# Performance work log

Hardware: AMD Instinct MI355X
Metric: run time of the kernel (lower is better)

## Reference

```python
import jax, jax.numpy as jnp
import numpy as np


def setup_inputs() -> dict:
    key = jax.random.key(0)
    ks = jax.random.split(key, 10)
    N, S, H = 500000, 128, 64
    s = lambda k, shape, fan_in: jax.random.normal(k, shape, dtype=jnp.float32) / np.sqrt(fan_in)
    return {
        "my_state": jax.random.normal(ks[0], (S,), dtype=jnp.float32),
        "neighbor_states": jax.random.normal(ks[1], (N, S), dtype=jnp.float32),
        "embed_w": s(ks[2], (S, H), S),
        "embed_b": s(ks[3], (H,), S),
        "key_w": s(ks[4], (H, H), H),
        "key_b": s(ks[5], (H,), H),
        "query_w": s(ks[6], (S + H, H), S + H),
        "query_b": s(ks[7], (H,), S + H),
        "attn_w": s(ks[8], (2 * H, 1), 2 * H),
        "attn_b": s(ks[9], (1,), 2 * H),
    }


def reference(my_state, neighbor_states, embed_w, embed_b, key_w, key_b,
              query_w, query_b, attn_w, attn_b):
    H = embed_w.shape[1]
    # per-neighbor embeddings and keys: [N, H]
    emb = neighbor_states @ embed_w + embed_b
    keys = emb @ key_w + key_b
    # query from own state + mean neighbor embedding: [H]
    mean_emb = emb.mean(axis=0)
    query = jnp.concatenate([my_state, mean_emb], axis=-1) @ query_w + query_b
    # attention_net(cat(query, key)) split so we never materialize [N, 2H]
    wq, wk = attn_w[:H, 0], attn_w[H:, 0]
    scores = keys @ wk + (query @ wq + attn_b[0])  # [N]
    attention_weights = jax.nn.softmax(scores, axis=0)  # [N]
    weighted_embedding = attention_weights @ emb  # [H]
    return weighted_embedding, attention_weights
```

## Files before the change

kernel.cpp:

```cpp
#include <hip/hip_runtime.h>
#include <math.h>


#define S_DIM 128
#define H_DIM 64
#define NBLK  2048

__global__ void k_precompute_u(const float* __restrict__ embed_w,
                               const float* __restrict__ key_w,
                               const float* __restrict__ attn_w,
                               float* __restrict__ u)
{
    __shared__ float kv[H_DIM];
    const int t = threadIdx.x;
    if (t < H_DIM) {
        float acc = 0.f;
        #pragma unroll 8
        for (int j = 0; j < H_DIM; ++j) acc += key_w[t * H_DIM + j] * attn_w[H_DIM + j];
        kv[t] = acc;
    }
    __syncthreads();
    float acc = 0.f;
    #pragma unroll 8
    for (int h = 0; h < H_DIM; ++h) acc += embed_w[t * H_DIM + h] * kv[h];
    u[t] = acc;
}

__global__ __launch_bounds__(256) void k_pass1(
    const float* __restrict__ X,
    const float* __restrict__ u,
    float* __restrict__ scores_out,
    float* __restrict__ pz,
    float* __restrict__ pt_t,
    int N)
{
    const int tid  = threadIdx.x;
    const int lane = tid & 63;
    const int li   = lane & 31;
    const int half = lane >> 5;
    const int w    = tid >> 6;

    const float4 u4 = *(const float4*)(u + 4 * li);

    const int pairs = (N + 1) >> 1;
    const int start = (int)(((long long)blockIdx.x       * pairs) / NBLK);
    const int end   = (int)(((long long)(blockIdx.x + 1) * pairs) / NBLK);

    auto loadp = [&](int p) -> float4 {
        int row = 2 * p + half;
        row = row < N ? row : N - 1;
        return *(const float4*)(X + (size_t)row * S_DIM + 4 * li);
    };

    float  Za = 0.f, Zb = 0.f;
    float4 ta = make_float4(0.f, 0.f, 0.f, 0.f);
    float4 tb = make_float4(0.f, 0.f, 0.f, 0.f);

    auto proc = [&](const float4& x, int p, float& Z, float4& t) {
        float pp = x.x * u4.x + x.y * u4.y + x.z * u4.z + x.w * u4.w;
        pp += __shfl_xor(pp, 1);
        pp += __shfl_xor(pp, 2);
        pp += __shfl_xor(pp, 4);
        pp += __shfl_xor(pp, 8);
        pp += __shfl_xor(pp, 16);
        const int  row = 2 * p + half;
        const bool v   = (p < end) && (row < N);
        if (li == 0 && v) scores_out[row] = pp;
        const float e = v ? __expf(pp) : 0.f;
        Z   += e;
        t.x += e * x.x;
        t.y += e * x.y;
        t.z += e * x.z;
        t.w += e * x.w;
    };

    int p = start + w;
    float4 xa = loadp(p);
    float4 xb = loadp(p + 4);
    while (p < end) {
        float4 na = loadp(p + 8);
        float4 nb = loadp(p + 12);
        proc(xa, p,     Za, ta);
        proc(xb, p + 4, Zb, tb);
        xa = na; xb = nb; p += 8;
    }

    const float  Z = Za + Zb;
    const float4 t = make_float4(ta.x + tb.x, ta.y + tb.y, ta.z + tb.z, ta.w + tb.w);

    __shared__ float sT[8][S_DIM];
    __shared__ float sZ[8];
    const int hs = w * 2 + half;
    sT[hs][4 * li + 0] = t.x;
    sT[hs][4 * li + 1] = t.y;
    sT[hs][4 * li + 2] = t.z;
    sT[hs][4 * li + 3] = t.w;
    if (li == 0) sZ[hs] = Z;
    __syncthreads();

    if (tid < S_DIM) {
        float acc = 0.f;
        #pragma unroll
        for (int h = 0; h < 8; ++h) acc += sT[h][tid];
        pt_t[(size_t)tid * NBLK + blockIdx.x] = acc;
    }
    if (tid == 0) {
        float z = 0.f;
        #pragma unroll
        for (int h = 0; h < 8; ++h) z += sZ[h];
        pz[blockIdx.x] = z;
    }
}

__global__ __launch_bounds__(256) void k_pass2(
    const float* __restrict__ pz, const float* __restrict__ pt_t,
    float* __restrict__ tS,
    float* __restrict__ zstar)
{
    const int k   = blockIdx.x;
    const int tid = threadIdx.x;
    __shared__ float red[256];

    float z = 0.f;
    for (int b = tid; b < NBLK; b += 256) z += pz[b];
    red[tid] = z; __syncthreads();
    for (int s = 128; s; s >>= 1) { if (tid < s) red[tid] += red[tid + s]; __syncthreads(); }
    const float Z = red[0]; __syncthreads();

    float tacc = 0.f;
    for (int b = tid; b < NBLK; b += 256) tacc += pt_t[(size_t)k * NBLK + b];
    red[tid] = tacc; __syncthreads();
    for (int s = 128; s; s >>= 1) { if (tid < s) red[tid] += red[tid + s]; __syncthreads(); }

    if (tid == 0) {
        tS[k] = red[0] / Z;
        if (k == 0) zstar[0] = Z;
    }
}

__global__ __launch_bounds__(256) void k_pass3(
    float* __restrict__ sw, const float* __restrict__ zstar,
    const float* __restrict__ tS, const float* __restrict__ embed_w,
    const float* __restrict__ embed_b, float* __restrict__ out_emb, int N)
{
    const int tid = threadIdx.x;
    if (blockIdx.x == 0) {
        if (tid < H_DIM) {
            float acc = embed_b[tid];
            #pragma unroll 8
            for (int k = 0; k < S_DIM; ++k) acc += tS[k] * embed_w[k * H_DIM + tid];
            out_emb[tid] = acc;
        } else if (tid == H_DIM) {
            const float invZ = 1.0f / zstar[0];
            for (int i = (N >> 2) << 2; i < N; ++i) sw[i] = __expf(sw[i]) * invZ;
        }
        return;
    }
    const float invZ = 1.0f / zstar[0];
    const int n4 = N >> 2;
    const int stride = (gridDim.x - 1) * 256;
    for (int i = (blockIdx.x - 1) * 256 + tid; i < n4; i += stride) {
        float4 v = ((float4*)sw)[i];
        v.x = __expf(v.x) * invZ;
        v.y = __expf(v.y) * invZ;
        v.z = __expf(v.z) * invZ;
        v.w = __expf(v.w) * invZ;
        ((float4*)sw)[i] = v;
    }
}

extern "C" void kernel_launch(void* const* d_in, const int* in_sizes, int n_in,
                              void* d_out, int out_size, void* d_ws, size_t ws_size,
                              hipStream_t stream) {
    const float* X       = (const float*)d_in[1];
    const float* embed_w = (const float*)d_in[2];
    const float* embed_b = (const float*)d_in[3];
    const float* key_w   = (const float*)d_in[4];
    const float* attn_w  = (const float*)d_in[8];
    float* out = (float*)d_out;

    const int N = in_sizes[1] / S_DIM;

    float* ws    = (float*)d_ws;
    float* zstar = ws;
    float* u     = ws + 64;
    float* tS    = ws + 192;
    float* pz    = ws + 320;
    float* pt_t  = pz + NBLK;

    float* out_emb = out;
    float* out_w   = out + H_DIM;

    k_precompute_u<<<1, 128, 0, stream>>>(embed_w, key_w, attn_w, u);
    k_pass1<<<NBLK, 256, 0, stream>>>(X, u, out_w, pz, pt_t, N);
    k_pass2<<<S_DIM, 256, 0, stream>>>(pz, pt_t, tS, zstar);
    const int nb3 = ((N >> 2) + 255) / 256 + 1;
    k_pass3<<<nb3, 256, 0, stream>>>(out_w, zstar, tS, embed_w, embed_b, out_emb, N);
}
```

Measured before the change: 64.89 us.

## Fuse u precompute into pass1 and process four rows per wave with nontemporal loads

Drops the single-block precompute kernel and has every pass1 block compute the projection vector u into shared memory, removing one launch and its serial dependency. The streaming loop now maps 16 lanes to each row (8 floats per lane), so a wave covers four rows per step. It uses nontemporal loads for the large neighbor matrix and reduces the per-row shuffle tree by one step. The cost is redundant u computation in all 2048 blocks (small weight reads, mostly cache hits) and a single prefetch stage instead of two.

```diff
diff --git a/kernel.cpp b/kernel.cpp
--- a/kernel.cpp
+++ b/kernel.cpp
@@ -2,114 +2,111 @@
 #include <math.h>
 
 
-#define S_DIM 128
-#define H_DIM 64
-#define NBLK  2048
+#define S_DIM  128
+#define H_DIM  64
+#define NBLK   2048
 
-__global__ void k_precompute_u(const float* __restrict__ embed_w,
-                               const float* __restrict__ key_w,
-                               const float* __restrict__ attn_w,
-                               float* __restrict__ u)
-{
-    __shared__ float kv[H_DIM];
-    const int t = threadIdx.x;
-    if (t < H_DIM) {
-        float acc = 0.f;
-        #pragma unroll 8
-        for (int j = 0; j < H_DIM; ++j) acc += key_w[t * H_DIM + j] * attn_w[H_DIM + j];
-        kv[t] = acc;
-    }
-    __syncthreads();
-    float acc = 0.f;
-    #pragma unroll 8
-    for (int h = 0; h < H_DIM; ++h) acc += embed_w[t * H_DIM + h] * kv[h];
-    u[t] = acc;
-}
+typedef float f4 __attribute__((ext_vector_type(4)));
 
 __global__ __launch_bounds__(256) void k_pass1(
     const float* __restrict__ X,
-    const float* __restrict__ u,
+    const float* __restrict__ embed_w,
+    const float* __restrict__ key_w,
+    const float* __restrict__ attn_w,
     float* __restrict__ scores_out,
     float* __restrict__ pz,
     float* __restrict__ pt_t,
     int N)
 {
-    const int tid  = threadIdx.x;
+    __shared__ float s_kv[H_DIM];
+    __shared__ float s_u[S_DIM];
+    __shared__ float sT[4][S_DIM];
+    __shared__ float sZ[4];
+
+    const int tid = threadIdx.x;
+
+    if (tid < H_DIM) {
+        float acc = 0.f;
+        #pragma unroll 8
+        for (int j = 0; j < H_DIM; ++j) acc += key_w[tid * H_DIM + j] * attn_w[H_DIM + j];
+        s_kv[tid] = acc;
+    }
+    __syncthreads();
+    if (tid < S_DIM) {
+        float acc = 0.f;
+        #pragma unroll 8
+        for (int h = 0; h < H_DIM; ++h) acc += embed_w[tid * H_DIM + h] * s_kv[h];
+        s_u[tid] = acc;
+    }
+    __syncthreads();
+
     const int lane = tid & 63;
-    const int li   = lane & 31;
-    const int half = lane >> 5;
     const int w    = tid >> 6;
+    const int l16  = lane & 15;
+    const int g    = lane >> 4;
 
-    const float4 u4 = *(const float4*)(u + 4 * li);
+    const f4 uLo = *(const f4*)(s_u + 8 * l16);
+    const f4 uHi = *(const f4*)(s_u + 8 * l16 + 4);
 
-    const int pairs = (N + 1) >> 1;
-    const int start = (int)(((long long)blockIdx.x       * pairs) / NBLK);
-    const int end   = (int)(((long long)(blockIdx.x + 1) * pairs) / NBLK);
+    const int quads = (N + 3) >> 2;
+    const int qs = (int)(((long long)blockIdx.x       * quads) / NBLK);
+    const int qe = (int)(((long long)(blockIdx.x + 1) * quads) / NBLK);
 
-    auto loadp = [&](int p) -> float4 {
-        int row = 2 * p + half;
+    auto loadrow = [&](int q, f4& lo, f4& hi) {
+        int row = 4 * q + g;
         row = row < N ? row : N - 1;
-        return *(const float4*)(X + (size_t)row * S_DIM + 4 * li);
+        const float* p = X + (size_t)row * S_DIM + 8 * l16;
+        lo = __builtin_nontemporal_load((const f4*)p);
+        hi = __builtin_nontemporal_load((const f4*)(p + 4));
     };
 
-    float  Za = 0.f, Zb = 0.f;
-    float4 ta = make_float4(0.f, 0.f, 0.f, 0.f);
-    float4 tb = make_float4(0.f, 0.f, 0.f, 0.f);
+    float Z  = 0.f;
+    f4 tLo = (f4)(0.f);
+    f4 tHi = (f4)(0.f);
 
-    auto proc = [&](const float4& x, int p, float& Z, float4& t) {
-        float pp = x.x * u4.x + x.y * u4.y + x.z * u4.z + x.w * u4.w;
-        pp += __shfl_xor(pp, 1);
-        pp += __shfl_xor(pp, 2);
-        pp += __shfl_xor(pp, 4);
-        pp += __shfl_xor(pp, 8);
-        pp += __shfl_xor(pp, 16);
-        const int  row = 2 * p + half;
-        const bool v   = (p < end) && (row < N);
-        if (li == 0 && v) scores_out[row] = pp;
-        const float e = v ? __expf(pp) : 0.f;
+    int q = qs + w;
+    f4 lo, hi;
+    loadrow(q, lo, hi);
+
+    while (q < qe) {
+        f4 nlo, nhi;
+        loadrow(q + 4, nlo, nhi);
+
+        float s8 = lo.x * uLo.x + lo.y * uLo.y + lo.z * uLo.z + lo.w * uLo.w
+                 + hi.x * uHi.x + hi.y * uHi.y + hi.z * uHi.z + hi.w * uHi.w;
+        s8 += __shfl_xor(s8, 1);
+        s8 += __shfl_xor(s8, 2);
+        s8 += __shfl_xor(s8, 4);
+        s8 += __shfl_xor(s8, 8);
+
+        const int  row = 4 * q + g;
+        const bool v   = row < N;
+        if (l16 == 0 && v) scores_out[row] = s8;
+
+        const float e = v ? __expf(s8) : 0.f;
         Z   += e;
-        t.x += e * x.x;
-        t.y += e * x.y;
-        t.z += e * x.z;
-        t.w += e * x.w;
-    };
+        tLo += e * lo;
+        tHi += e * hi;
 
-    int p = start + w;
-    float4 xa = loadp(p);
-    float4 xb = loadp(p + 4);
-    while (p < end) {
-        float4 na = loadp(p + 8);
-        float4 nb = loadp(p + 12);
-        proc(xa, p,     Za, ta);
-        proc(xb, p + 4, Zb, tb);
-        xa = na; xb = nb; p += 8;
+        lo = nlo; hi = nhi; q += 4;
     }
 
-    const float  Z = Za + Zb;
-    const float4 t = make_float4(ta.x + tb.x, ta.y + tb.y, ta.z + tb.z, ta.w + tb.w);
+    auto red2 = [](float v) { v += __shfl_xor(v, 16); v += __shfl_xor(v, 32); return v; };
+    tLo.x = red2(tLo.x); tLo.y = red2(tLo.y); tLo.z = red2(tLo.z); tLo.w = red2(tLo.w);
+    tHi.x = red2(tHi.x); tHi.y = red2(tHi.y); tHi.z = red2(tHi.z); tHi.w = red2(tHi.w);
+    Z = red2(Z);
 
-    __shared__ float sT[8][S_DIM];
-    __shared__ float sZ[8];
-    const int hs = w * 2 + half;
-    sT[hs][4 * li + 0] = t.x;
-    sT[hs][4 * li + 1] = t.y;
-    sT[hs][4 * li + 2] = t.z;
-    sT[hs][4 * li + 3] = t.w;
-    if (li == 0) sZ[hs] = Z;
+    if (lane < 16) {
+        *(f4*)(&sT[w][8 * l16])     = tLo;
+        *(f4*)(&sT[w][8 * l16 + 4]) = tHi;
+    }
+    if (lane == 0) sZ[w] = Z;
     __syncthreads();
 
-    if (tid < S_DIM) {
-        float acc = 0.f;
-        #pragma unroll
-        for (int h = 0; h < 8; ++h) acc += sT[h][tid];
-        pt_t[(size_t)tid * NBLK + blockIdx.x] = acc;
-    }
-    if (tid == 0) {
-        float z = 0.f;
-        #pragma unroll
-        for (int h = 0; h < 8; ++h) z += sZ[h];
-        pz[blockIdx.x] = z;
-    }
+    if (tid < S_DIM)
+        pt_t[(size_t)tid * NBLK + blockIdx.x] = sT[0][tid] + sT[1][tid] + sT[2][tid] + sT[3][tid];
+    else if (tid == S_DIM)
+        pz[blockIdx.x] = sZ[0] + sZ[1] + sZ[2] + sZ[3];
 }
 
 __global__ __launch_bounds__(256) void k_pass2(
@@ -160,12 +157,12 @@
     const int n4 = N >> 2;
     const int stride = (gridDim.x - 1) * 256;
     for (int i = (blockIdx.x - 1) * 256 + tid; i < n4; i += stride) {
-        float4 v = ((float4*)sw)[i];
+        f4 v = ((f4*)sw)[i];
         v.x = __expf(v.x) * invZ;
         v.y = __expf(v.y) * invZ;
         v.z = __expf(v.z) * invZ;
         v.w = __expf(v.w) * invZ;
-        ((float4*)sw)[i] = v;
+        ((f4*)sw)[i] = v;
     }
 }
 
@@ -183,16 +180,14 @@
 
     float* ws    = (float*)d_ws;
     float* zstar = ws;
-    float* u     = ws + 64;
-    float* tS    = ws + 192;
-    float* pz    = ws + 320;
+    float* tS    = ws + 64;
+    float* pz    = ws + 256;
     float* pt_t  = pz + NBLK;
 
     float* out_emb = out;
     float* out_w   = out + H_DIM;
 
-    k_precompute_u<<<1, 128, 0, stream>>>(embed_w, key_w, attn_w, u);
-    k_pass1<<<NBLK, 256, 0, stream>>>(X, u, out_w, pz, pt_t, N);
+    k_pass1<<<NBLK, 256, 0, stream>>>(X, embed_w, key_w, attn_w, out_w, pz, pt_t, N);
     k_pass2<<<S_DIM, 256, 0, stream>>>(pz, pt_t, tS, zstar);
     const int nb3 = ((N >> 2) + 255) / 256 + 1;
     k_pass3<<<nb3, 256, 0, stream>>>(out_w, zstar, tS, embed_w, embed_b, out_emb, N);
```

After: 81.70 us. 1.26x slower.

## Fuse precompute into stream kernel and merge reduction passes into one final kernel

Applied to the files above, without the earlier changes.

Each of the 2048 streaming blocks now recomputes the u vector itself, so the separate single-block precompute launch goes away. The streaming kernel stores exp(score) instead of the raw score, and projects its partial S-space sum through embed_w to H-space before writing it out. Two launches remain instead of four: the final kernel normalizes the weights with multiplies only, no exp, and reduces 64 H-dim partials instead of 128. In exchange, every block does the small u and projection matmuls redundantly, and the result relies on the exp values not overflowing, since no max is subtracted, as in the code before.

```diff
diff --git a/kernel.cpp b/kernel.cpp
--- a/kernel.cpp
+++ b/kernel.cpp
@@ -5,58 +5,64 @@
 #define S_DIM 128
 #define H_DIM 64
 #define NBLK  2048
+#define NB2   512
 
-__global__ void k_precompute_u(const float* __restrict__ embed_w,
-                               const float* __restrict__ key_w,
-                               const float* __restrict__ attn_w,
-                               float* __restrict__ u)
+typedef float f4 __attribute__((ext_vector_type(4)));
+
+__global__ __launch_bounds__(256) void k_stream(
+    const float* __restrict__ X,
+    const float* __restrict__ embed_w,
+    const float* __restrict__ key_w,
+    const float* __restrict__ attn_w,
+    float* __restrict__ e_out,
+    float* __restrict__ pz,
+    float* __restrict__ pv_t,
+    int N)
 {
-    __shared__ float kv[H_DIM];
-    const int t = threadIdx.x;
-    if (t < H_DIM) {
+    __shared__ float s_kv[H_DIM];
+    __shared__ float s_u[S_DIM];
+    __shared__ float sT[8][S_DIM];
+    __shared__ float sZ[8];
+    __shared__ float red[256];
+
+    const int tid = threadIdx.x;
+
+    if (tid < H_DIM) {
         float acc = 0.f;
         #pragma unroll 8
-        for (int j = 0; j < H_DIM; ++j) acc += key_w[t * H_DIM + j] * attn_w[H_DIM + j];
-        kv[t] = acc;
+        for (int j = 0; j < H_DIM; ++j) acc += key_w[tid * H_DIM + j] * attn_w[H_DIM + j];
+        s_kv[tid] = acc;
     }
     __syncthreads();
-    float acc = 0.f;
-    #pragma unroll 8
-    for (int h = 0; h < H_DIM; ++h) acc += embed_w[t * H_DIM + h] * kv[h];
-    u[t] = acc;
-}
+    if (tid < S_DIM) {
+        float acc = 0.f;
+        #pragma unroll 8
+        for (int h = 0; h < H_DIM; ++h) acc += embed_w[tid * H_DIM + h] * s_kv[h];
+        s_u[tid] = acc;
+    }
+    __syncthreads();
 
-__global__ __launch_bounds__(256) void k_pass1(
-    const float* __restrict__ X,
-    const float* __restrict__ u,
-    float* __restrict__ scores_out,
-    float* __restrict__ pz,
-    float* __restrict__ pt_t,
-    int N)
-{
-    const int tid  = threadIdx.x;
     const int lane = tid & 63;
     const int li   = lane & 31;
     const int half = lane >> 5;
     const int w    = tid >> 6;
 
-    const float4 u4 = *(const float4*)(u + 4 * li);
+    const f4 u4 = *(const f4*)(s_u + 4 * li);
 
     const int pairs = (N + 1) >> 1;
     const int start = (int)(((long long)blockIdx.x       * pairs) / NBLK);
     const int end   = (int)(((long long)(blockIdx.x + 1) * pairs) / NBLK);
 
-    auto loadp = [&](int p) -> float4 {
+    auto loadp = [&](int p) -> f4 {
         int row = 2 * p + half;
         row = row < N ? row : N - 1;
-        return *(const float4*)(X + (size_t)row * S_DIM + 4 * li);
+        return *(const f4*)(X + (size_t)row * S_DIM + 4 * li);
     };
 
-    float  Za = 0.f, Zb = 0.f;
-    float4 ta = make_float4(0.f, 0.f, 0.f, 0.f);
-    float4 tb = make_float4(0.f, 0.f, 0.f, 0.f);
+    float Za = 0.f, Zb = 0.f;
+    f4 ta = (f4)(0.f), tb = (f4)(0.f);
 
-    auto proc = [&](const float4& x, int p, float& Z, float4& t) {
+    auto proc = [&](const f4& x, int p, float& Z, f4& t) {
         float pp = x.x * u4.x + x.y * u4.y + x.z * u4.z + x.w * u4.w;
         pp += __shfl_xor(pp, 1);
         pp += __shfl_xor(pp, 2);
@@ -65,107 +71,86 @@
         pp += __shfl_xor(pp, 16);
         const int  row = 2 * p + half;
         const bool v   = (p < end) && (row < N);
-        if (li == 0 && v) scores_out[row] = pp;
-        const float e = v ? __expf(pp) : 0.f;
-        Z   += e;
-        t.x += e * x.x;
-        t.y += e * x.y;
-        t.z += e * x.z;
-        t.w += e * x.w;
+        const float e  = v ? __expf(pp) : 0.f;
+        if (li == 0 && v) e_out[row] = e;
+        Z += e;
+        t += e * x;
     };
 
     int p = start + w;
-    float4 xa = loadp(p);
-    float4 xb = loadp(p + 4);
+    f4 xa = loadp(p);
+    f4 xb = loadp(p + 4);
     while (p < end) {
-        float4 na = loadp(p + 8);
-        float4 nb = loadp(p + 12);
+        f4 na = loadp(p + 8);
+        f4 nb = loadp(p + 12);
         proc(xa, p,     Za, ta);
         proc(xb, p + 4, Zb, tb);
         xa = na; xb = nb; p += 8;
     }
 
-    const float  Z = Za + Zb;
-    const float4 t = make_float4(ta.x + tb.x, ta.y + tb.y, ta.z + tb.z, ta.w + tb.w);
+    const float Z = Za + Zb;
+    const f4    t = ta + tb;
 
-    __shared__ float sT[8][S_DIM];
-    __shared__ float sZ[8];
     const int hs = w * 2 + half;
-    sT[hs][4 * li + 0] = t.x;
-    sT[hs][4 * li + 1] = t.y;
-    sT[hs][4 * li + 2] = t.z;
-    sT[hs][4 * li + 3] = t.w;
+    *(f4*)(&sT[hs][4 * li]) = t;
     if (li == 0) sZ[hs] = Z;
     __syncthreads();
 
-    if (tid < S_DIM) {
+    if (tid < S_DIM)
+        s_u[tid] = sT[0][tid] + sT[1][tid] + sT[2][tid] + sT[3][tid]
+                 + sT[4][tid] + sT[5][tid] + sT[6][tid] + sT[7][tid];
+    if (tid == 0)
+        pz[blockIdx.x] = sZ[0] + sZ[1] + sZ[2] + sZ[3] + sZ[4] + sZ[5] + sZ[6] + sZ[7];
+    __syncthreads();
+
+    {
+        const int h = tid & 63, q4 = tid >> 6;
         float acc = 0.f;
-        #pragma unroll
-        for (int h = 0; h < 8; ++h) acc += sT[h][tid];
-        pt_t[(size_t)tid * NBLK + blockIdx.x] = acc;
-    }
-    if (tid == 0) {
-        float z = 0.f;
-        #pragma unroll
-        for (int h = 0; h < 8; ++h) z += sZ[h];
-        pz[blockIdx.x] = z;
+        #pragma unroll 8
+        for (int k = 32 * q4; k < 32 * q4 + 32; ++k)
+            acc += s_u[k] * embed_w[k * H_DIM + h];
+        red[tid] = acc;
+        __syncthreads();
+        if (tid < H_DIM)
+            pv_t[(size_t)tid * NBLK + blockIdx.x] =
+                red[tid] + red[tid + 64] + red[tid + 128] + red[tid + 192];
     }
 }
 
-__global__ __launch_bounds__(256) void k_pass2(
-    const float* __restrict__ pz, const float* __restrict__ pt_t,
-    float* __restrict__ tS,
-    float* __restrict__ zstar)
+__global__ __launch_bounds__(256) void k_final(
+    float* __restrict__ sw,
+    const float* __restrict__ pz,
+    const float* __restrict__ pv_t,
+    const float* __restrict__ embed_b,
+    float* __restrict__ out_emb,
+    int N)
 {
-    const int k   = blockIdx.x;
+    __shared__ float red[256];
     const int tid = threadIdx.x;
-    __shared__ float red[256];
+    const int bid = blockIdx.x;
 
     float z = 0.f;
-    for (int b = tid; b < NBLK; b += 256) z += pz[b];
+    for (int i = tid; i < NBLK; i += 256) z += pz[i];
     red[tid] = z; __syncthreads();
     for (int s = 128; s; s >>= 1) { if (tid < s) red[tid] += red[tid + s]; __syncthreads(); }
-    const float Z = red[0]; __syncthreads();
+    const float invZ = 1.0f / red[0];
+    __syncthreads();
 
-    float tacc = 0.f;
-    for (int b = tid; b < NBLK; b += 256) tacc += pt_t[(size_t)k * NBLK + b];
-    red[tid] = tacc; __syncthreads();
-    for (int s = 128; s; s >>= 1) { if (tid < s) red[tid] += red[tid + s]; __syncthreads(); }
+    const int n4 = N >> 2;
+    for (int i = bid * 256 + tid; i < n4; i += NB2 * 256) {
+        f4 v = ((f4*)sw)[i];
+        v *= invZ;
+        ((f4*)sw)[i] = v;
+    }
+    if (bid == 0 && tid == 0)
+        for (int i = n4 << 2; i < N; ++i) sw[i] *= invZ;
 
-    if (tid == 0) {
-        tS[k] = red[0] / Z;
-        if (k == 0) zstar[0] = Z;
-    }
-}
-
-__global__ __launch_bounds__(256) void k_pass3(
-    float* __restrict__ sw, const float* __restrict__ zstar,
-    const float* __restrict__ tS, const float* __restrict__ embed_w,
-    const float* __restrict__ embed_b, float* __restrict__ out_emb, int N)
-{
-    const int tid = threadIdx.x;
-    if (blockIdx.x == 0) {
-        if (tid < H_DIM) {
-            float acc = embed_b[tid];
-            #pragma unroll 8
-            for (int k = 0; k < S_DIM; ++k) acc += tS[k] * embed_w[k * H_DIM + tid];
-            out_emb[tid] = acc;
-        } else if (tid == H_DIM) {
-            const float invZ = 1.0f / zstar[0];
-            for (int i = (N >> 2) << 2; i < N; ++i) sw[i] = __expf(sw[i]) * invZ;
-        }
-        return;
-    }
-    const float invZ = 1.0f / zstar[0];
-    const int n4 = N >> 2;
-    const int stride = (gridDim.x - 1) * 256;
-    for (int i = (blockIdx.x - 1) * 256 + tid; i < n4; i += stride) {
-        float4 v = ((float4*)sw)[i];
-        v.x = __expf(v.x) * invZ;
-        v.y = __expf(v.y) * invZ;
-        v.z = __expf(v.z) * invZ;
-        v.w = __expf(v.w) * invZ;
-        ((float4*)sw)[i] = v;
+    if (bid < H_DIM) {
+        float a = 0.f;
+        for (int i = tid; i < NBLK; i += 256) a += pv_t[(size_t)bid * NBLK + i];
+        red[tid] = a; __syncthreads();
+        for (int s = 128; s; s >>= 1) { if (tid < s) red[tid] += red[tid + s]; __syncthreads(); }
+        if (tid == 0) out_emb[bid] = red[0] * invZ + embed_b[bid];
     }
 }
 
@@ -181,19 +166,12 @@
 
     const int N = in_sizes[1] / S_DIM;
 
-    float* ws    = (float*)d_ws;
-    float* zstar = ws;
-    float* u     = ws + 64;
-    float* tS    = ws + 192;
-    float* pz    = ws + 320;
-    float* pt_t  = pz + NBLK;
+    float* pz   = (float*)d_ws;
+    float* pv_t = pz + NBLK;
 
     float* out_emb = out;
     float* out_w   = out + H_DIM;
 
-    k_precompute_u<<<1, 128, 0, stream>>>(embed_w, key_w, attn_w, u);
-    k_pass1<<<NBLK, 256, 0, stream>>>(X, u, out_w, pz, pt_t, N);
-    k_pass2<<<S_DIM, 256, 0, stream>>>(pz, pt_t, tS, zstar);
-    const int nb3 = ((N >> 2) + 255) / 256 + 1;
-    k_pass3<<<nb3, 256, 0, stream>>>(out_w, zstar, tS, embed_w, embed_b, out_emb, N);
+    k_stream<<<NBLK, 256, 0, stream>>>(X, embed_w, key_w, attn_w, out_w, pz, pv_t, N);
+    k_final<<<NB2, 256, 0, stream>>>(out_w, pz, pv_t, embed_b, out_emb, N);
 }
```

Result: no change. 63.83 us (-1.6%).
